# Performance work log

Measured on AMD Instinct MI355X. Metric: run time of the kernel, lower is better.

The kernel has to match this reference:

```python
import jax, jax.numpy as jnp
import numpy as np

NUM_HEADS = 16


def setup_inputs() -> dict:
    key = jax.random.key(0)
    ks = jax.random.split(key, 7)
    B, S, D = 2, 2048, 1024
    scale = 1.0 / np.sqrt(D)
    return {
        "queries": jax.random.normal(ks[0], (B, S, D), jnp.float32),
        "keys": jax.random.normal(ks[1], (B, S, D), jnp.float32),
        "values": jax.random.normal(ks[2], (B, S, D), jnp.float32),
        "Wq": jax.random.normal(ks[3], (D, D), jnp.float32) * scale,
        "Wk": jax.random.normal(ks[4], (D, D), jnp.float32) * scale,
        "Wv": jax.random.normal(ks[5], (D, D), jnp.float32) * scale,
        "Wo": jax.random.normal(ks[6], (D, D), jnp.float32) * scale,
    }


def _split_heads(x, h):
    # [B, S, D] -> [B, h, S, D/h]
    B, S, D = x.shape
    return x.reshape(B, S, h, D // h).transpose(0, 2, 1, 3)


def reference(queries, keys, values, Wq, Wk, Wv, Wo):
    h = NUM_HEADS
    q = _split_heads(queries @ Wq, h)  # [B, h, S, dh]
    k = _split_heads(keys @ Wk, h)
    v = _split_heads(values @ Wv, h)
    dh = q.shape[-1]
    scores = jnp.einsum("bhqd,bhkd->bhqk", q, k) / jnp.sqrt(jnp.float32(dh))
    attn = jax.nn.softmax(scores, axis=-1)
    y = jnp.einsum("bhqk,bhkd->bhqd", attn, v)  # [B, h, S, dh]
    B, _, S, _ = y.shape
    y = y.transpose(0, 2, 1, 3).reshape(B, S, h * dh)
    return y @ Wo
```

## Files before the change

kernel.cpp:

```cpp
#include <hip/hip_runtime.h>
#include <hip/hip_bf16.h>


typedef __attribute__((ext_vector_type(8))) short bf16x8;
typedef __attribute__((ext_vector_type(4))) float f32x4;
typedef __attribute__((ext_vector_type(16))) float f32x16;
typedef __attribute__((ext_vector_type(4))) unsigned int u32x4;

#define QSCALE 0.18033688011112042f

__device__ __forceinline__ unsigned short f2b(float f) {
    unsigned int u = __float_as_uint(f);
    u += 0x7FFFu + ((u >> 16) & 1u);
    return (unsigned short)(u >> 16);
}

__device__ __forceinline__ float b2f(unsigned short s) {
    return __uint_as_float((unsigned int)s << 16);
}

__device__ __forceinline__ unsigned cvt_pk_bf16(float lo, float hi) {
    unsigned r;
    asm("v_cvt_pk_bf16_f32 %0, %1, %2" : "=v"(r) : "v"(lo), "v"(hi));
    return r;
}

__device__ __forceinline__ void gld_lds16(const void* g, void* l) {
    __builtin_amdgcn_global_load_lds(
        (const __attribute__((address_space(1))) unsigned int*)g,
        (__attribute__((address_space(3))) unsigned int*)l, 16, 0, 0);
}

__global__ __launch_bounds__(256) void f32_to_bf16_3(
    const float* __restrict__ i0, const float* __restrict__ i1, const float* __restrict__ i2,
    unsigned short* __restrict__ o0, unsigned short* __restrict__ o1, unsigned short* __restrict__ o2)
{
    const int z = blockIdx.y;
    const float* in = z == 0 ? i0 : (z == 1 ? i1 : i2);
    unsigned short* out = z == 0 ? o0 : (z == 1 ? o1 : o2);
    int i = blockIdx.x * 256 + threadIdx.x;
    float4 v = ((const float4*)in)[i];
    ushort4 o;
    o.x = f2b(v.x); o.y = f2b(v.y); o.z = f2b(v.z); o.w = f2b(v.w);
    ((ushort4*)out)[i] = o;
}

__global__ __launch_bounds__(256) void transpose_w4(
    const float* __restrict__ W0, const float* __restrict__ W1,
    const float* __restrict__ W2, const float* __restrict__ W3,
    unsigned short* __restrict__ O0, unsigned short* __restrict__ O1,
    unsigned short* __restrict__ O2, unsigned short* __restrict__ O3)
{
    __shared__ unsigned short tile[32][33];
    const int z = blockIdx.z;
    const float* in = z == 0 ? W0 : z == 1 ? W1 : z == 2 ? W2 : W3;
    unsigned short* out = z == 0 ? O0 : z == 1 ? O1 : z == 2 ? O2 : O3;
    const int c0 = blockIdx.x * 32, r0 = blockIdx.y * 32;
    const int tx = threadIdx.x, ty = threadIdx.y;
#pragma unroll
    for (int i = 0; i < 4; ++i)
        tile[ty + i * 8][tx] = f2b(in[(size_t)(r0 + ty + i * 8) * 1024 + c0 + tx]);
    __syncthreads();
#pragma unroll
    for (int i = 0; i < 4; ++i)
        out[(size_t)(c0 + ty + i * 8) * 1024 + r0 + tx] = tile[tx][ty + i * 8];
}

template <int BN, int MODE>
__global__ __launch_bounds__(256) void gemm_bt(
    const unsigned short* __restrict__ A0, const unsigned short* __restrict__ A1,
    const unsigned short* __restrict__ A2,
    const unsigned short* __restrict__ B0, const unsigned short* __restrict__ B1,
    const unsigned short* __restrict__ B2,
    void* __restrict__ Cq, void* __restrict__ Ck, void* __restrict__ Cv)
{
    constexpr int K = 1024, N = 1024;
    constexpr int NB = BN / 32;
    __shared__ unsigned short lds_a[2][128 * 32];
    __shared__ unsigned short lds_b[2][BN * 32];
    const int tid = threadIdx.x;
    const int wid = tid >> 6, ln = tid & 15, lg = (tid & 63) >> 4;
    const int z = (MODE == 1) ? blockIdx.z : 0;
    const unsigned short* A = (z == 0) ? A0 : (z == 1) ? A1 : A2;
    const unsigned short* Bt = (z == 0) ? B0 : (z == 1) ? B1 : B2;
    const int m0 = blockIdx.y * 128, n0 = blockIdx.x * BN;
    const int wr = wid >> 1, wc = wid & 1;

    f32x4 acc[4][NB];
#pragma unroll
    for (int m = 0; m < 4; ++m)
#pragma unroll
        for (int n = 0; n < NB; ++n) acc[m][n] = {};

    const unsigned short* ga = A + (size_t)(m0 + (tid >> 2)) * K + (tid & 3) * 8;
    const unsigned short* gb = Bt + (size_t)(n0 + (tid >> 2)) * K + (tid & 3) * 8;

    auto stage = [&](int buf, int k0) {
        gld_lds16(ga + k0, &lds_a[buf][wid * 512]);
        gld_lds16(ga + k0 + 64 * K, &lds_a[buf][wid * 512 + 2048]);
        gld_lds16(gb + k0, &lds_b[buf][wid * 512]);
        if constexpr (BN == 128) gld_lds16(gb + k0 + 64 * K, &lds_b[buf][wid * 512 + 2048]);
    };

    stage(0, 0);
    __syncthreads();

    for (int k0 = 0; k0 < K; k0 += 32) {
        const int buf = (k0 >> 5) & 1;
        if (k0 + 32 < K) stage(buf ^ 1, k0 + 32);

        bf16x8 af[4], bfr[NB];
#pragma unroll
        for (int m = 0; m < 4; ++m)
            af[m] = *(const bf16x8*)&lds_a[buf][(wr * 64 + m * 16 + ln) * 32 + lg * 8];
#pragma unroll
        for (int n = 0; n < NB; ++n)
            bfr[n] = *(const bf16x8*)&lds_b[buf][(wc * (BN / 2) + n * 16 + ln) * 32 + lg * 8];
#pragma unroll
        for (int m = 0; m < 4; ++m)
#pragma unroll
            for (int n = 0; n < NB; ++n)
                acc[m][n] = __builtin_amdgcn_mfma_f32_16x16x32_bf16(af[m], bfr[n], acc[m][n], 0, 0, 0);
        __syncthreads();
    }

    const int gcb = n0 + wc * (BN / 2) + ln;
    const int grb = m0 + wr * 64 + lg * 4;

    if constexpr (MODE == 0) {
        float* C = (float*)Cq;
#pragma unroll
        for (int m = 0; m < 4; ++m)
#pragma unroll
            for (int n = 0; n < NB; ++n)
#pragma unroll
                for (int r = 0; r < 4; ++r)
                    C[(size_t)(grb + m * 16 + r) * N + gcb + n * 16] = acc[m][n][r];
    } else {
        if (z == 0) {
            unsigned short* C = (unsigned short*)Cq;
#pragma unroll
            for (int m = 0; m < 4; ++m)
#pragma unroll
                for (int n = 0; n < NB; ++n)
#pragma unroll
                    for (int r = 0; r < 4; ++r)
                        C[(size_t)(grb + m * 16 + r) * N + gcb + n * 16] =
                            f2b(acc[m][n][r] * QSCALE);
        } else if (z == 1) {
            unsigned short* Kp = (unsigned short*)Ck;
#pragma unroll
            for (int m = 0; m < 4; ++m)
#pragma unroll
                for (int n = 0; n < NB; ++n) {
                    int gr = grb + m * 16, gc = gcb + n * 16;
                    int bq = gr >> 11, kvg = gr & 2047, kvt = kvg >> 6;
                    int h = gc >> 6, d = gc & 63;
                    size_t img = ((size_t)(bq * 16 + h) * 32 + kvt) * 4096;
                    int ks = d >> 4, hib = (d >> 3) & 1, i = d & 7;
                    int kvb = kvg & 63, T = kvb >> 5;
                    size_t base = img + T * 2048 + ks * 512 + hib * 256 + i;
#pragma unroll
                    for (int r = 0; r < 4; ++r)
                        Kp[base + ((kvb & 31) + r) * 8] = f2b(acc[m][n][r]);
                }
        } else {
            unsigned short* Vp = (unsigned short*)Cv;
#pragma unroll
            for (int m = 0; m < 4; ++m)
#pragma unroll
                for (int n = 0; n < NB; ++n) {
                    int gr = grb + m * 16, gc = gcb + n * 16;
                    int bq = gr >> 11, kvg = gr & 2047, kvt = kvg >> 6;
                    int h = gc >> 6, d = gc & 63;
                    size_t img = ((size_t)(bq * 16 + h) * 32 + kvt) * 4096;
                    int kvb = kvg & 63;
                    int T = kvb >> 5, g = (kvb >> 3) & 3, hib = (kvb >> 2) & 1;
                    int kstep = 2 * T + (g >> 1);
                    int dt = d >> 5, ln31 = d & 31;
                    size_t addr = img + dt * 2048 + kstep * 512 + hib * 256 + ln31 * 8 + (g & 1) * 4;
                    uint2 w;
                    w.x = cvt_pk_bf16(acc[m][n][0], acc[m][n][1]);
                    w.y = cvt_pk_bf16(acc[m][n][2], acc[m][n][3]);
                    *(uint2*)(Vp + addr) = w;
                }
        }
    }
}

__global__ __launch_bounds__(64, 4) void attn_kernel(
    const unsigned short* __restrict__ Qp,
    const unsigned short* __restrict__ Kpack,
    const unsigned short* __restrict__ Vpack,
    unsigned short* __restrict__ Opart,
    float2* __restrict__ ML)
{
    const int lane = threadIdx.x;
    const int q31 = lane & 31, hi = lane >> 5;

    const int logical = (blockIdx.x & 7) * 512 + (blockIdx.x >> 3);
    const int qb = logical & 63, rest = logical >> 6;
    const int bh = rest & 31, s = rest >> 5;
    const int b = bh >> 4, h = bh & 15;
    const int q0 = qb * 32;

    const unsigned short* qrow = Qp + (size_t)(b * 2048 + q0 + q31) * 1024 + h * 64 + hi * 8;
    bf16x8 qf[4];
#pragma unroll
    for (int ks = 0; ks < 4; ++ks) qf[ks] = *(const bf16x8*)(qrow + ks * 16);

    const unsigned short* gk = Kpack + (size_t)bh * (32 * 4096) + lane * 8;
    const unsigned short* gv = Vpack + (size_t)bh * (32 * 4096) + lane * 8;

    float m_run = -1e30f, l_run = 0.f;
    f32x16 o[2] = {{}, {}};

    for (int kvt = s * 16; kvt < s * 16 + 16; ++kvt) {
        const size_t tb = (size_t)kvt * 4096;

        f32x16 st[2];
#pragma unroll
        for (int T = 0; T < 2; ++T) {
            f32x16 zacc = {};
#pragma unroll
            for (int ks = 0; ks < 4; ++ks) {
                bf16x8 ka = *(const bf16x8*)(gk + tb + T * 2048 + ks * 512);
                zacc = __builtin_amdgcn_mfma_f32_32x32x16_bf16(ka, qf[ks], zacc, 0, 0, 0);
            }
            st[T] = zacc;
        }

        float a0 = fmaxf(fmaxf(st[0][0], st[0][1]), st[0][2]);
        float a1 = fmaxf(fmaxf(st[0][3], st[0][4]), st[0][5]);
        float a2 = fmaxf(fmaxf(st[0][6], st[0][7]), st[0][8]);
        float a3 = fmaxf(fmaxf(st[0][9], st[0][10]), st[0][11]);
        float a4 = fmaxf(fmaxf(st[0][12], st[0][13]), st[0][14]);
        float a5 = fmaxf(fmaxf(st[0][15], st[1][0]), st[1][1]);
        float a6 = fmaxf(fmaxf(st[1][2], st[1][3]), st[1][4]);
        float a7 = fmaxf(fmaxf(st[1][5], st[1][6]), st[1][7]);
        float a8 = fmaxf(fmaxf(st[1][8], st[1][9]), st[1][10]);
        float a9 = fmaxf(fmaxf(st[1][11], st[1][12]), st[1][13]);
        float aa = fmaxf(st[1][14], st[1][15]);
        a0 = fmaxf(fmaxf(a0, a1), a2);
        a3 = fmaxf(fmaxf(a3, a4), a5);
        a6 = fmaxf(fmaxf(a6, a7), a8);
        a9 = fmaxf(a9, aa);
        float pm = fmaxf(fmaxf(a0, a3), fmaxf(a6, a9));
        pm = fmaxf(pm, __shfl_xor(pm, 32));

        float mn;
        bool skip = __all(pm - m_run <= 8.f);
        if (skip) {
            mn = m_run;
        } else {
            mn = fmaxf(m_run, pm);
            const float alpha = __builtin_amdgcn_exp2f(m_run - mn);
            m_run = mn;
            l_run *= alpha;
#pragma unroll
            for (int r = 0; r < 16; ++r) { o[0][r] *= alpha; o[1][r] *= alpha; }
        }

        float rs = 0.f;
        unsigned pk[2][8];
#pragma unroll
        for (int T = 0; T < 2; ++T)
#pragma unroll
            for (int g = 0; g < 4; ++g) {
                float p0 = __builtin_amdgcn_exp2f(st[T][g * 4 + 0] - mn);
                float p1 = __builtin_amdgcn_exp2f(st[T][g * 4 + 1] - mn);
                float p2 = __builtin_amdgcn_exp2f(st[T][g * 4 + 2] - mn);
                float p3 = __builtin_amdgcn_exp2f(st[T][g * 4 + 3] - mn);
                rs += (p0 + p1) + (p2 + p3);
                pk[T][g * 2 + 0] = cvt_pk_bf16(p0, p1);
                pk[T][g * 2 + 1] = cvt_pk_bf16(p2, p3);
            }
        rs += __shfl_xor(rs, 32);
        l_run += rs;

#pragma unroll
        for (int dt = 0; dt < 2; ++dt)
#pragma unroll
            for (int kstep = 0; kstep < 4; ++kstep) {
                bf16x8 va = *(const bf16x8*)(gv + tb + dt * 2048 + kstep * 512);
                u32x4 w = {pk[kstep >> 1][4 * (kstep & 1) + 0], pk[kstep >> 1][4 * (kstep & 1) + 1],
                           pk[kstep >> 1][4 * (kstep & 1) + 2], pk[kstep >> 1][4 * (kstep & 1) + 3]};
                o[dt] = __builtin_amdgcn_mfma_f32_32x32x16_bf16(
                    va, __builtin_bit_cast(bf16x8, w), o[dt], 0, 0, 0);
            }
    }

    unsigned short* op = Opart + ((size_t)(s * 32 + bh) * 2048 + q0 + q31) * 64 + hi * 4;
#pragma unroll
    for (int dt = 0; dt < 2; ++dt)
#pragma unroll
        for (int g = 0; g < 4; ++g) {
            uint2 w;
            w.x = cvt_pk_bf16(o[dt][g * 4 + 0], o[dt][g * 4 + 1]);
            w.y = cvt_pk_bf16(o[dt][g * 4 + 2], o[dt][g * 4 + 3]);
            *(uint2*)(op + dt * 32 + g * 8) = w;
        }
    if (hi == 0)
        ML[(size_t)(s * 32 + bh) * 2048 + q0 + q31] = make_float2(m_run, l_run);
}

__global__ __launch_bounds__(256) void attn_combine(
    const unsigned short* __restrict__ Opart,
    const float2* __restrict__ ML,
    unsigned short* __restrict__ Y)
{
    const int gq = blockIdx.x * 16 + (threadIdx.x >> 4);
    const int l16 = threadIdx.x & 15;
    const int bh = gq >> 11, q = gq & 2047;
    const int b = bh >> 4, h = bh & 15;

    const size_t r0 = ((size_t)bh * 2048 + q) * 64 + l16 * 4;
    const size_t r1 = ((size_t)(32 + bh) * 2048 + q) * 64 + l16 * 4;
    ushort4 u0 = *(const ushort4*)(Opart + r0);
    ushort4 u1 = *(const ushort4*)(Opart + r1);
    float2 ml0 = ML[(size_t)bh * 2048 + q];
    float2 ml1 = ML[(size_t)(32 + bh) * 2048 + q];

    const float m = fmaxf(ml0.x, ml1.x);
    float w0 = __builtin_amdgcn_exp2f(ml0.x - m);
    float w1 = __builtin_amdgcn_exp2f(ml1.x - m);
    const float inv = __builtin_amdgcn_rcpf(ml0.y * w0 + ml1.y * w1);
    w0 *= inv; w1 *= inv;

    uint2 w;
    w.x = cvt_pk_bf16(b2f(u0.x) * w0 + b2f(u1.x) * w1,
                      b2f(u0.y) * w0 + b2f(u1.y) * w1);
    w.y = cvt_pk_bf16(b2f(u0.z) * w0 + b2f(u1.z) * w1,
                      b2f(u0.w) * w0 + b2f(u1.w) * w1);
    *(uint2*)(Y + (size_t)(b * 2048 + q) * 1024 + h * 64 + l16 * 4) = w;
}

extern "C" void kernel_launch(void* const* d_in, const int* in_sizes, int n_in,
                              void* d_out, int out_size, void* d_ws, size_t ws_size,
                              hipStream_t stream)
{
    const float* q_f = (const float*)d_in[0];
    const float* k_f = (const float*)d_in[1];
    const float* v_f = (const float*)d_in[2];
    const float* Wq  = (const float*)d_in[3];
    const float* Wk  = (const float*)d_in[4];
    const float* Wv  = (const float*)d_in[5];
    const float* Wo  = (const float*)d_in[6];
    float* out = (float*)d_out;

    const size_t X = (size_t)4096 * 1024;
    const size_t W = (size_t)1024 * 1024;
    unsigned short* ws  = (unsigned short*)d_ws;
    unsigned short* qb  = ws;
    unsigned short* kb  = qb + X;
    unsigned short* vb  = kb + X;
    unsigned short* wqt = vb + X;
    unsigned short* wkt = wqt + W;
    unsigned short* wvt = wkt + W;
    unsigned short* wot = wvt + W;
    unsigned short* Qp  = wot + W;
    unsigned short* Kpk = Qp + X;
    unsigned short* Vpk = Kpk + X;
    unsigned short* Yb  = Vpk + X;
    unsigned short* Opart = qb;
    float2*         ML    = (float2*)vb;

    f32_to_bf16_3<<<dim3(4096, 3), 256, 0, stream>>>(q_f, k_f, v_f, qb, kb, vb);
    transpose_w4<<<dim3(32, 32, 4), dim3(32, 8), 0, stream>>>(Wq, Wk, Wv, Wo,
                                                              wqt, wkt, wvt, wot);
    gemm_bt<128, 1><<<dim3(8, 32, 3), 256, 0, stream>>>(qb, kb, vb, wqt, wkt, wvt,
                                                        Qp, Kpk, Vpk);
    attn_kernel<<<4096, 64, 0, stream>>>(Qp, Kpk, Vpk, Opart, ML);
    attn_combine<<<4096, 256, 0, stream>>>(Opart, ML, Yb);
    gemm_bt<64, 0><<<dim3(16, 32, 1), 256, 0, stream>>>(Yb, nullptr, nullptr,
                                                        wot, nullptr, nullptr,
                                                        out, nullptr, nullptr);
}
```

Baseline: 247.1 us.

## Use 256x256 QKV GEMM, separate K repack, drop attention split-KV combine

Replaces the QKV projection with a 512-thread 256x256-tile GEMM using swizzled LDS, a 64-wide K step and MFMA priority hints. K is now written row-major and repacked by a separate kernel. The attention kernel no longer splits the KV range in two: each block covers all 32 KV tiles, prefetches K and V fragments into registers, and normalizes and writes Y directly, so the combine kernel goes away. The trade-off is half as many attention blocks with longer serial loops and higher register pressure, plus an extra repack pass over K.

```diff
diff --git a/kernel.cpp b/kernel.cpp
--- a/kernel.cpp
+++ b/kernel.cpp
@@ -13,10 +13,6 @@
     unsigned int u = __float_as_uint(f);
     u += 0x7FFFu + ((u >> 16) & 1u);
     return (unsigned short)(u >> 16);
-}
-
-__device__ __forceinline__ float b2f(unsigned short s) {
-    return __uint_as_float((unsigned int)s << 16);
 }
 
 __device__ __forceinline__ unsigned cvt_pk_bf16(float lo, float hi) {
@@ -66,13 +62,150 @@
         out[(size_t)(c0 + ty + i * 8) * 1024 + r0 + tx] = tile[tx][ty + i * 8];
 }
 
-template <int BN, int MODE>
-__global__ __launch_bounds__(256) void gemm_bt(
+__device__ __forceinline__ void vpack_store(unsigned short* Vp, int gr, int gc,
+                                            const f32x4& a)
+{
+    int bq = gr >> 11, kvg = gr & 2047, kvt = kvg >> 6;
+    int h = gc >> 6, d = gc & 63;
+    size_t img = ((size_t)(bq * 16 + h) * 32 + kvt) * 4096;
+    int kvb = kvg & 63;
+    int T = kvb >> 5, g = (kvb >> 3) & 3, hib = (kvb >> 2) & 1;
+    int kstep = 2 * T + (g >> 1);
+    int dt = d >> 5, ln31 = d & 31;
+    size_t addr = img + dt * 2048 + kstep * 512 + hib * 256 + ln31 * 8 + (g & 1) * 4;
+    uint2 w;
+    w.x = cvt_pk_bf16(a[0], a[1]);
+    w.y = cvt_pk_bf16(a[2], a[3]);
+    *(uint2*)(Vp + addr) = w;
+}
+
+__device__ __forceinline__ int lds_fragaddr(int slot, int mat, int half, int row,
+                                            int ks, int lg)
+{
+    int c8s = lg ^ ((row >> 1) & 3);
+    return slot * 32768 + mat * 16384 + half * 8192 +
+           (((row >> 4) * 2 + ks) * 512) + (row & 15) * 32 + c8s * 8;
+}
+
+__global__ __launch_bounds__(512, 2) void gemm256(
     const unsigned short* __restrict__ A0, const unsigned short* __restrict__ A1,
     const unsigned short* __restrict__ A2,
     const unsigned short* __restrict__ B0, const unsigned short* __restrict__ B1,
     const unsigned short* __restrict__ B2,
-    void* __restrict__ Cq, void* __restrict__ Ck, void* __restrict__ Cv)
+    unsigned short* __restrict__ Cq,
+    unsigned short* __restrict__ Ckrm,
+    unsigned short* __restrict__ Cv)
+{
+    __shared__ unsigned short lds[65536];
+    const int tid = threadIdx.x;
+    const int wid = tid >> 6, ln = tid & 15, lg = (tid & 63) >> 4;
+    const int wr = wid >> 2, wc = wid & 3;
+    const int z = blockIdx.z;
+    const unsigned short* A = (z == 0) ? A0 : (z == 1) ? A1 : A2;
+    const unsigned short* Bt = (z == 0) ? B0 : (z == 1) ? B1 : B2;
+    const int m0 = blockIdx.y * 256, n0 = blockIdx.x * 256;
+
+    f32x4 acc[8][4];
+#pragma unroll
+    for (int m = 0; m < 8; ++m)
+#pragma unroll
+        for (int n = 0; n < 4; ++n) acc[m][n] = {};
+
+    const unsigned short* srcA[2][2];
+    const unsigned short* srcB[2][2];
+#pragma unroll
+    for (int j = 0; j < 2; ++j) {
+        const int ci = tid + j * 512;
+        const int s = ci >> 6, r16 = (ci >> 2) & 15, c8 = ci & 3;
+        const int c8s = c8 ^ ((r16 >> 1) & 3);
+        const int rih = (s >> 1) * 16 + r16;
+        const int colc = (s & 1) * 4 + c8s;
+#pragma unroll
+        for (int half = 0; half < 2; ++half) {
+            srcA[j][half] = A + (size_t)(m0 + half * 128 + rih) * 1024 + colc * 8;
+            srcB[j][half] = Bt + (size_t)(n0 + half * 128 + rih) * 1024 + colc * 8;
+        }
+    }
+
+    auto stage = [&](int slot, int k0) {
+#pragma unroll
+        for (int j = 0; j < 2; ++j) {
+            const int ci = tid + j * 512;
+#pragma unroll
+            for (int half = 0; half < 2; ++half) {
+                gld_lds16(srcA[j][half] + k0,
+                          &lds[slot * 32768 + half * 8192 + ci * 8]);
+                gld_lds16(srcB[j][half] + k0,
+                          &lds[slot * 32768 + 16384 + half * 8192 + ci * 8]);
+            }
+        }
+    };
+
+    stage(0, 0);
+    __syncthreads();
+
+    for (int t = 0; t < 16; ++t) {
+        const int slot = t & 1;
+        if (t < 15) stage(slot ^ 1, (t + 1) * 64);
+
+#pragma unroll
+        for (int qd = 0; qd < 4; ++qd) {
+            const int mh = qd >> 1, nh = qd & 1;
+            bf16x8 af[4][2], bfr[2][2];
+#pragma unroll
+            for (int mm = 0; mm < 4; ++mm)
+#pragma unroll
+                for (int ks = 0; ks < 2; ++ks)
+                    af[mm][ks] = *(const bf16x8*)&lds[
+                        lds_fragaddr(slot, 0, wr, (mh * 4 + mm) * 16 + ln, ks, lg)];
+#pragma unroll
+            for (int nn = 0; nn < 2; ++nn)
+#pragma unroll
+                for (int ks = 0; ks < 2; ++ks)
+                    bfr[nn][ks] = *(const bf16x8*)&lds[
+                        lds_fragaddr(slot, 1, wc >> 1,
+                                     (wc & 1) * 64 + (nh * 2 + nn) * 16 + ln, ks, lg)];
+            __builtin_amdgcn_s_setprio(1);
+#pragma unroll
+            for (int mm = 0; mm < 4; ++mm)
+#pragma unroll
+                for (int nn = 0; nn < 2; ++nn)
+#pragma unroll
+                    for (int ks = 0; ks < 2; ++ks)
+                        acc[mh * 4 + mm][nh * 2 + nn] =
+                            __builtin_amdgcn_mfma_f32_16x16x32_bf16(
+                                af[mm][ks], bfr[nn][ks],
+                                acc[mh * 4 + mm][nh * 2 + nn], 0, 0, 0);
+            __builtin_amdgcn_s_setprio(0);
+        }
+        __syncthreads();
+    }
+
+#pragma unroll
+    for (int m = 0; m < 8; ++m)
+#pragma unroll
+        for (int n = 0; n < 4; ++n) {
+            const int gr = m0 + wr * 128 + m * 16 + lg * 4;
+            const int gc = n0 + wc * 64 + n * 16 + ln;
+            if (z == 0) {
+#pragma unroll
+                for (int r = 0; r < 4; ++r)
+                    Cq[(size_t)(gr + r) * 1024 + gc] = f2b(acc[m][n][r] * QSCALE);
+            } else if (z == 1) {
+#pragma unroll
+                for (int r = 0; r < 4; ++r)
+                    Ckrm[(size_t)(gr + r) * 1024 + gc] = f2b(acc[m][n][r]);
+            } else {
+                vpack_store(Cv, gr, gc, acc[m][n]);
+            }
+        }
+}
+
+template <int BN, int MODE>
+__global__ __launch_bounds__(256) void gemm_bt(
+    const unsigned short* __restrict__ A0,
+    const unsigned short* __restrict__ B0,
+    void* __restrict__ Cq)
 {
     constexpr int K = 1024, N = 1024;
     constexpr int NB = BN / 32;
@@ -80,9 +213,8 @@
     __shared__ unsigned short lds_b[2][BN * 32];
     const int tid = threadIdx.x;
     const int wid = tid >> 6, ln = tid & 15, lg = (tid & 63) >> 4;
-    const int z = (MODE == 1) ? blockIdx.z : 0;
-    const unsigned short* A = (z == 0) ? A0 : (z == 1) ? A1 : A2;
-    const unsigned short* Bt = (z == 0) ? B0 : (z == 1) ? B1 : B2;
+    const unsigned short* A = A0;
+    const unsigned short* Bt = B0;
     const int m0 = blockIdx.y * 128, n0 = blockIdx.x * BN;
     const int wr = wid >> 1, wc = wid & 1;
 
@@ -126,81 +258,43 @@
 
     const int gcb = n0 + wc * (BN / 2) + ln;
     const int grb = m0 + wr * 64 + lg * 4;
-
-    if constexpr (MODE == 0) {
-        float* C = (float*)Cq;
-#pragma unroll
-        for (int m = 0; m < 4; ++m)
-#pragma unroll
-            for (int n = 0; n < NB; ++n)
-#pragma unroll
-                for (int r = 0; r < 4; ++r)
-                    C[(size_t)(grb + m * 16 + r) * N + gcb + n * 16] = acc[m][n][r];
-    } else {
-        if (z == 0) {
-            unsigned short* C = (unsigned short*)Cq;
-#pragma unroll
-            for (int m = 0; m < 4; ++m)
-#pragma unroll
-                for (int n = 0; n < NB; ++n)
-#pragma unroll
-                    for (int r = 0; r < 4; ++r)
-                        C[(size_t)(grb + m * 16 + r) * N + gcb + n * 16] =
-                            f2b(acc[m][n][r] * QSCALE);
-        } else if (z == 1) {
-            unsigned short* Kp = (unsigned short*)Ck;
-#pragma unroll
-            for (int m = 0; m < 4; ++m)
-#pragma unroll
-                for (int n = 0; n < NB; ++n) {
-                    int gr = grb + m * 16, gc = gcb + n * 16;
-                    int bq = gr >> 11, kvg = gr & 2047, kvt = kvg >> 6;
-                    int h = gc >> 6, d = gc & 63;
-                    size_t img = ((size_t)(bq * 16 + h) * 32 + kvt) * 4096;
-                    int ks = d >> 4, hib = (d >> 3) & 1, i = d & 7;
-                    int kvb = kvg & 63, T = kvb >> 5;
-                    size_t base = img + T * 2048 + ks * 512 + hib * 256 + i;
-#pragma unroll
-                    for (int r = 0; r < 4; ++r)
-                        Kp[base + ((kvb & 31) + r) * 8] = f2b(acc[m][n][r]);
-                }
-        } else {
-            unsigned short* Vp = (unsigned short*)Cv;
-#pragma unroll
-            for (int m = 0; m < 4; ++m)
-#pragma unroll
-                for (int n = 0; n < NB; ++n) {
-                    int gr = grb + m * 16, gc = gcb + n * 16;
-                    int bq = gr >> 11, kvg = gr & 2047, kvt = kvg >> 6;
-                    int h = gc >> 6, d = gc & 63;
-                    size_t img = ((size_t)(bq * 16 + h) * 32 + kvt) * 4096;
-                    int kvb = kvg & 63;
-                    int T = kvb >> 5, g = (kvb >> 3) & 3, hib = (kvb >> 2) & 1;
-                    int kstep = 2 * T + (g >> 1);
-                    int dt = d >> 5, ln31 = d & 31;
-                    size_t addr = img + dt * 2048 + kstep * 512 + hib * 256 + ln31 * 8 + (g & 1) * 4;
-                    uint2 w;
-                    w.x = cvt_pk_bf16(acc[m][n][0], acc[m][n][1]);
-                    w.y = cvt_pk_bf16(acc[m][n][2], acc[m][n][3]);
-                    *(uint2*)(Vp + addr) = w;
-                }
-        }
+    float* C = (float*)Cq;
+#pragma unroll
+    for (int m = 0; m < 4; ++m)
+#pragma unroll
+        for (int n = 0; n < NB; ++n)
+#pragma unroll
+            for (int r = 0; r < 4; ++r)
+                C[(size_t)(grb + m * 16 + r) * N + gcb + n * 16] = acc[m][n][r];
+}
+
+__global__ __launch_bounds__(256) void k_repack(
+    const unsigned short* __restrict__ Krm, unsigned short* __restrict__ Kp)
+{
+    const int kvt = blockIdx.x, bh = blockIdx.y;
+    const int bq = bh >> 4, h = bh & 15;
+    const int tid = threadIdx.x;
+    const int kvr = tid & 31, hib = (tid >> 5) & 1, ks = (tid >> 6) & 3;
+    const size_t img = ((size_t)bh * 32 + kvt) * 4096;
+#pragma unroll
+    for (int T = 0; T < 2; ++T) {
+        const int row = bq * 2048 + kvt * 64 + T * 32 + kvr;
+        bf16x8 v = *(const bf16x8*)&Krm[(size_t)row * 1024 + h * 64 + ks * 16 + hib * 8];
+        *(bf16x8*)&Kp[img + T * 2048 + ks * 512 + hib * 256 + kvr * 8] = v;
     }
 }
 
-__global__ __launch_bounds__(64, 4) void attn_kernel(
+__global__ __launch_bounds__(64) void attn_kernel(
     const unsigned short* __restrict__ Qp,
     const unsigned short* __restrict__ Kpack,
     const unsigned short* __restrict__ Vpack,
-    unsigned short* __restrict__ Opart,
-    float2* __restrict__ ML)
+    unsigned short* __restrict__ Y)
 {
     const int lane = threadIdx.x;
     const int q31 = lane & 31, hi = lane >> 5;
 
-    const int logical = (blockIdx.x & 7) * 512 + (blockIdx.x >> 3);
-    const int qb = logical & 63, rest = logical >> 6;
-    const int bh = rest & 31, s = rest >> 5;
+    const int logical = (blockIdx.x & 7) * 256 + (blockIdx.x >> 3);
+    const int qb = logical & 63, bh = logical >> 6;
     const int b = bh >> 4, h = bh & 15;
     const int q0 = qb * 32;
 
@@ -215,19 +309,31 @@
     float m_run = -1e30f, l_run = 0.f;
     f32x16 o[2] = {{}, {}};
 
-    for (int kvt = s * 16; kvt < s * 16 + 16; ++kvt) {
+    bf16x8 ka[8];
+#pragma unroll
+    for (int f = 0; f < 8; ++f) ka[f] = *(const bf16x8*)(gk + f * 512);
+
+    for (int kvt = 0; kvt < 32; ++kvt) {
         const size_t tb = (size_t)kvt * 4096;
+
+        bf16x8 va[8];
+#pragma unroll
+        for (int f = 0; f < 8; ++f) va[f] = *(const bf16x8*)(gv + tb + f * 512);
 
         f32x16 st[2];
 #pragma unroll
         for (int T = 0; T < 2; ++T) {
             f32x16 zacc = {};
 #pragma unroll
-            for (int ks = 0; ks < 4; ++ks) {
-                bf16x8 ka = *(const bf16x8*)(gk + tb + T * 2048 + ks * 512);
-                zacc = __builtin_amdgcn_mfma_f32_32x32x16_bf16(ka, qf[ks], zacc, 0, 0, 0);
-            }
+            for (int ks = 0; ks < 4; ++ks)
+                zacc = __builtin_amdgcn_mfma_f32_32x32x16_bf16(ka[T * 4 + ks], qf[ks], zacc, 0, 0, 0);
             st[T] = zacc;
+        }
+
+        if (kvt < 31) {
+#pragma unroll
+            for (int f = 0; f < 8; ++f)
+                ka[f] = *(const bf16x8*)(gk + tb + 4096 + f * 512);
         }
 
         float a0 = fmaxf(fmaxf(st[0][0], st[0][1]), st[0][2]);
@@ -282,57 +388,24 @@
         for (int dt = 0; dt < 2; ++dt)
 #pragma unroll
             for (int kstep = 0; kstep < 4; ++kstep) {
-                bf16x8 va = *(const bf16x8*)(gv + tb + dt * 2048 + kstep * 512);
                 u32x4 w = {pk[kstep >> 1][4 * (kstep & 1) + 0], pk[kstep >> 1][4 * (kstep & 1) + 1],
                            pk[kstep >> 1][4 * (kstep & 1) + 2], pk[kstep >> 1][4 * (kstep & 1) + 3]};
                 o[dt] = __builtin_amdgcn_mfma_f32_32x32x16_bf16(
-                    va, __builtin_bit_cast(bf16x8, w), o[dt], 0, 0, 0);
+                    va[dt * 4 + kstep], __builtin_bit_cast(bf16x8, w), o[dt], 0, 0, 0);
             }
     }
 
-    unsigned short* op = Opart + ((size_t)(s * 32 + bh) * 2048 + q0 + q31) * 64 + hi * 4;
+    const float inv = __builtin_amdgcn_rcpf(l_run);
+    unsigned short* yout = Y + (size_t)(b * 2048 + q0 + q31) * 1024 + h * 64 + hi * 4;
 #pragma unroll
     for (int dt = 0; dt < 2; ++dt)
 #pragma unroll
         for (int g = 0; g < 4; ++g) {
             uint2 w;
-            w.x = cvt_pk_bf16(o[dt][g * 4 + 0], o[dt][g * 4 + 1]);
-            w.y = cvt_pk_bf16(o[dt][g * 4 + 2], o[dt][g * 4 + 3]);
-            *(uint2*)(op + dt * 32 + g * 8) = w;
-        }
-    if (hi == 0)
-        ML[(size_t)(s * 32 + bh) * 2048 + q0 + q31] = make_float2(m_run, l_run);
-}
-
-__global__ __launch_bounds__(256) void attn_combine(
-    const unsigned short* __restrict__ Opart,
-    const float2* __restrict__ ML,
-    unsigned short* __restrict__ Y)
-{
-    const int gq = blockIdx.x * 16 + (threadIdx.x >> 4);
-    const int l16 = threadIdx.x & 15;
-    const int bh = gq >> 11, q = gq & 2047;
-    const int b = bh >> 4, h = bh & 15;
-
-    const size_t r0 = ((size_t)bh * 2048 + q) * 64 + l16 * 4;
-    const size_t r1 = ((size_t)(32 + bh) * 2048 + q) * 64 + l16 * 4;
-    ushort4 u0 = *(const ushort4*)(Opart + r0);
-    ushort4 u1 = *(const ushort4*)(Opart + r1);
-    float2 ml0 = ML[(size_t)bh * 2048 + q];
-    float2 ml1 = ML[(size_t)(32 + bh) * 2048 + q];
-
-    const float m = fmaxf(ml0.x, ml1.x);
-    float w0 = __builtin_amdgcn_exp2f(ml0.x - m);
-    float w1 = __builtin_amdgcn_exp2f(ml1.x - m);
-    const float inv = __builtin_amdgcn_rcpf(ml0.y * w0 + ml1.y * w1);
-    w0 *= inv; w1 *= inv;
-
-    uint2 w;
-    w.x = cvt_pk_bf16(b2f(u0.x) * w0 + b2f(u1.x) * w1,
-                      b2f(u0.y) * w0 + b2f(u1.y) * w1);
-    w.y = cvt_pk_bf16(b2f(u0.z) * w0 + b2f(u1.z) * w1,
-                      b2f(u0.w) * w0 + b2f(u1.w) * w1);
-    *(uint2*)(Y + (size_t)(b * 2048 + q) * 1024 + h * 64 + l16 * 4) = w;
+            w.x = cvt_pk_bf16(o[dt][g * 4 + 0] * inv, o[dt][g * 4 + 1] * inv);
+            w.y = cvt_pk_bf16(o[dt][g * 4 + 2] * inv, o[dt][g * 4 + 3] * inv);
+            *(uint2*)(yout + dt * 32 + g * 8) = w;
+        }
 }
 
 extern "C" void kernel_launch(void* const* d_in, const int* in_sizes, int n_in,
@@ -362,17 +435,17 @@
     unsigned short* Kpk = Qp + X;
     unsigned short* Vpk = Kpk + X;
     unsigned short* Yb  = Vpk + X;
-    unsigned short* Opart = qb;
-    float2*         ML    = (float2*)vb;
+    unsigned short* Krm = Yb;
 
     f32_to_bf16_3<<<dim3(4096, 3), 256, 0, stream>>>(q_f, k_f, v_f, qb, kb, vb);
     transpose_w4<<<dim3(32, 32, 4), dim3(32, 8), 0, stream>>>(Wq, Wk, Wv, Wo,
                                                               wqt, wkt, wvt, wot);
-    gemm_bt<128, 1><<<dim3(8, 32, 3), 256, 0, stream>>>(qb, kb, vb, wqt, wkt, wvt,
-                                                        Qp, Kpk, Vpk);
-    attn_kernel<<<4096, 64, 0, stream>>>(Qp, Kpk, Vpk, Opart, ML);
-    attn_combine<<<4096, 256, 0, stream>>>(Opart, ML, Yb);
-    gemm_bt<64, 0><<<dim3(16, 32, 1), 256, 0, stream>>>(Yb, nullptr, nullptr,
-                                                        wot, nullptr, nullptr,
-                                                        out, nullptr, nullptr);
-}
+
+    gemm256<<<dim3(4, 16, 3), 512, 0, stream>>>(qb, kb, vb, wqt, wkt, wvt,
+                                                Qp, Krm, Vpk);
+    k_repack<<<dim3(32, 32), 256, 0, stream>>>(Krm, Kpk);
+
+    attn_kernel<<<2048, 64, 0, stream>>>(Qp, Kpk, Vpk, Yb);
+
+    gemm_bt<64, 0><<<dim3(16, 32), 256, 0, stream>>>(Yb, wot, out);
+}
```

Measured after the change: 228.7 us. -7.4%, faster.
